# Kernel tuning notes

Measured on AMD Instinct MI355X. Metric: run time of the kernel, lower is better.

## Reference

```python
import jax, jax.numpy as jnp
import numpy as np

LN_EPS = 1e-5

def _layernorm(x, g, b):
    mu = jnp.mean(x, axis=-1, keepdims=True)
    var = jnp.mean(jnp.square(x - mu), axis=-1, keepdims=True)
    return (x - mu) * jax.lax.rsqrt(var + LN_EPS) * g + b

def setup_inputs() -> dict:
    key = jax.random.key(0)
    B, IN_DIM, S, D = 16384, 512, 32, 128
    ks = jax.random.split(key, 6)
    return {
        "x": jax.random.normal(ks[0], (B, IN_DIM), dtype=jnp.float32),
        "memory": jax.random.normal(ks[1], (1, S, D), dtype=jnp.float32),
        "ln_g": jnp.ones((IN_DIM,), dtype=jnp.float32),
        "ln_b": jnp.zeros((IN_DIM,), dtype=jnp.float32),
        "w_in": jax.random.normal(ks[2], (IN_DIM, D), dtype=jnp.float32) * 0.02,
        "b_in": jnp.zeros((D,), dtype=jnp.float32),
        "w_gate": jax.random.normal(ks[3], (2 * D, D), dtype=jnp.float32) * 0.02,
        "b_gate": jnp.zeros((D,), dtype=jnp.float32),
    }

def reference(x, memory, ln_g, ln_b, w_in, b_in, w_gate, b_gate):
    B = x.shape[0]
    mem = memory[0]                                   # [S, D]
    S, D = mem.shape
    x_proj = _layernorm(x, ln_g, ln_b) @ w_in + b_in  # [B, D]
    scores = x_proj @ mem.T                           # [B, S]
    probs = jax.nn.softmax(scores, axis=-1)           # [B, S]
    # read path
    read_content = probs @ mem                        # [B, D]
    # write path
    mem_b = jnp.broadcast_to(mem, (B, S, D))
    xp_b = jnp.broadcast_to(x_proj[:, None, :], (B, S, D))
    gate_in = jnp.concatenate([mem_b, xp_b], axis=-1)              # [B, S, 2D]
    update_gate = jax.nn.sigmoid(gate_in @ w_gate + b_gate)        # [B, S, D]
    write_info = probs[:, :, None] * x_proj[:, None, :]            # [B, S, D]
    avg_gate = jnp.mean(update_gate, axis=0, keepdims=True)        # [1, S, D]
    avg_write = jnp.mean(write_info, axis=0, keepdims=True)        # [1, S, D]
    new_memory = memory * (1.0 - avg_gate) + avg_write * avg_gate  # [1, S, D]
    return read_content, jax.lax.stop_gradient(new_memory)
```

## Files before the change

kernel.cpp:

```cpp
#include <hip/hip_runtime.h>
#include <hip/hip_bf16.h>
#include <stdint.h>

typedef __attribute__((ext_vector_type(8))) short bfrag_t;
typedef __attribute__((ext_vector_type(4))) float floatx4;
typedef __attribute__((ext_vector_type(8))) unsigned short ushort8_t;

#define WFRAG_OFF   0
#define GB_OFF      294912
#define BU_OFF      311296
#define BS_OFF      311808
#define MEMFRAG_OFF 311936
#define ACC_OFF     327680
#define NBLK        512

#define M_A     0
#define M_XPF   32768
#define M_U     40960
#define M_SC    57344
#define M_PR    61440
#define M_PRT   63488
#define M_LDS   65536

__device__ __forceinline__ unsigned short f2bf(float f) {
    union { __hip_bfloat16 b; unsigned short u; } cv;
    cv.b = __float2bfloat16(f);
    return cv.u;
}
__device__ __forceinline__ float bf2f(unsigned short h) {
    return __uint_as_float(((unsigned)h) << 16);
}
__device__ __forceinline__ void writefrag(unsigned short* wf, int k, int n, float v) {
    int kt = k >> 5, kk = k & 31;
    int lane = (n & 15) | ((kk >> 3) << 4);
    wf[(((kt * 18) + (n >> 4)) * 64 + lane) * 8 + (kk & 7)] = f2bf(v);
}

__global__ __launch_bounds__(256) void prep_kernel(
    const float* __restrict__ memv, const float* __restrict__ w_in,
    const float* __restrict__ b_in, const float* __restrict__ w_gate,
    const float* __restrict__ b_gate, unsigned char* __restrict__ ws)
{
    int bid = blockIdx.x, t = threadIdx.x;
    unsigned short* wfrag = (unsigned short*)(ws + WFRAG_OFF);
    const float* wg2 = w_gate + 128 * 128;

    if (bid < 256) {
        __shared__ float wrow[2][128];
        int k0 = bid * 2;
        wrow[t >> 7][t & 127] = w_in[(size_t)(k0 + (t >> 7)) * 128 + (t & 127)];
        __syncthreads();
        for (int kl = 0; kl < 2; ++kl) {
            int k = k0 + kl;
            float v;
            if (t < 128) {
                v = wrow[kl][t];
            } else {
                int d = t - 128;
                float acc = 0.f;
                #pragma unroll 16
                for (int j = 0; j < 128; ++j) acc += wrow[kl][j] * wg2[j * 128 + d];
                v = acc;
            }
            writefrag(wfrag, k, t, v);
            if (t < 32) {
                float acc = 0.f;
                #pragma unroll 16
                for (int d = 0; d < 128; ++d) acc += wrow[kl][d] * memv[t * 128 + d];
                writefrag(wfrag, k, 256 + t, acc);
            }
        }
    } else if (bid < 272) {
        int idx = (bid - 256) * 256 + t;
        int s = idx >> 7, d = idx & 127;
        float acc = b_gate[d];
        #pragma unroll 16
        for (int k = 0; k < 128; ++k) acc += memv[s * 128 + k] * w_gate[k * 128 + d];
        ((float*)(ws + GB_OFF))[idx] = acc;
    } else {
        if (t < 128) {
            float acc = 0.f;
            #pragma unroll 16
            for (int j = 0; j < 128; ++j) acc += b_in[j] * wg2[j * 128 + t];
            ((float*)(ws + BU_OFF))[t] = acc;
        }
        if (t < 32) {
            float acc = 0.f;
            #pragma unroll 16
            for (int d = 0; d < 128; ++d) acc += b_in[d] * memv[t * 128 + d];
            ((float*)(ws + BS_OFF))[t] = acc;
        }
        unsigned short* mfr = (unsigned short*)(ws + MEMFRAG_OFF);
        for (int idx = t; idx < 4096; idx += 256) {
            int s = idx >> 7, d = idx & 127;
            mfr[((d >> 4) * 64 + ((d & 15) | (((s >> 3) & 3) << 4))) * 8 + (s & 7)]
                = f2bf(memv[idx]);
        }
    }
}

__global__ __launch_bounds__(512, 4) void main_kernel(
    const float* __restrict__ x,
    const float* __restrict__ ln_g, const float* __restrict__ ln_b,
    const float* __restrict__ b_in, unsigned char* __restrict__ ws,
    float* __restrict__ out)
{
    __shared__ char smem[M_LDS] __attribute__((aligned(16)));

    int tid = threadIdx.x;
    int w = tid >> 6, l = tid & 63;
    int lane_lo = l & 15, lane_hi = l >> 4;
    int row_base = blockIdx.x * 32;

    int nf = (w < 2) ? 3 : 2;
    int nts[3] = {w, w + 8, 16 + w};
    const bfrag_t* wf = (const bfrag_t*)(ws + WFRAG_OFF);

    const float4* x4 = (const float4*)x;
    float4 g0 = ((const float4*)ln_g)[l];
    float4 g1 = ((const float4*)ln_g)[l + 64];
    float4 q0 = ((const float4*)ln_b)[l];
    float4 q1 = ((const float4*)ln_b)[l + 64];

    float4 xa[4], xb[4];
    #pragma unroll
    for (int i = 0; i < 4; ++i) {
        int r = w * 4 + i;
        xa[i] = x4[(size_t)(row_base + r) * 128 + l];
        xb[i] = x4[(size_t)(row_base + r) * 128 + 64 + l];
    }

    bfrag_t bcur[3], bnxt[3], bfar[3];
    #pragma unroll
    for (int i = 0; i < 3; ++i) {
        if (i < nf) {
            bcur[i] = wf[(0 * 18 + nts[i]) * 64 + l];
            bnxt[i] = wf[(1 * 18 + nts[i]) * 64 + l];
        }
    }
    float bin_v = b_in[w * 16 + lane_lo];
    float bu_v  = ((const float*)(ws + BU_OFF))[w * 16 + lane_lo];
    float bs_v  = (w < 2) ? ((const float*)(ws + BS_OFF))[w * 16 + lane_lo] : 0.f;

    #pragma unroll
    for (int i = 0; i < 4; ++i) {
        int r = w * 4 + i;
        float s1 = xa[i].x + xa[i].y + xa[i].z + xa[i].w + xb[i].x + xb[i].y + xb[i].z + xb[i].w;
        float s2 = xa[i].x*xa[i].x + xa[i].y*xa[i].y + xa[i].z*xa[i].z + xa[i].w*xa[i].w
                 + xb[i].x*xb[i].x + xb[i].y*xb[i].y + xb[i].z*xb[i].z + xb[i].w*xb[i].w;
        #pragma unroll
        for (int m = 1; m < 64; m <<= 1) {
            s1 += __shfl_xor(s1, m);
            s2 += __shfl_xor(s2, m);
        }
        float mu = s1 * (1.f / 512.f);
        float var = s2 * (1.f / 512.f) - mu * mu;
        float rs = rsqrtf(var + 1e-5f);
        float ya0 = (xa[i].x - mu) * rs * g0.x + q0.x;
        float ya1 = (xa[i].y - mu) * rs * g0.y + q0.y;
        float ya2 = (xa[i].z - mu) * rs * g0.z + q0.z;
        float ya3 = (xa[i].w - mu) * rs * g0.w + q0.w;
        float yb0 = (xb[i].x - mu) * rs * g1.x + q1.x;
        float yb1 = (xb[i].y - mu) * rs * g1.y + q1.y;
        float yb2 = (xb[i].z - mu) * rs * g1.z + q1.z;
        float yb3 = (xb[i].w - mu) * rs * g1.w + q1.w;
        unsigned long long pa =
            (unsigned long long)f2bf(ya0) | ((unsigned long long)f2bf(ya1) << 16) |
            ((unsigned long long)f2bf(ya2) << 32) | ((unsigned long long)f2bf(ya3) << 48);
        unsigned long long pb =
            (unsigned long long)f2bf(yb0) | ((unsigned long long)f2bf(yb1) << 16) |
            ((unsigned long long)f2bf(yb2) << 32) | ((unsigned long long)f2bf(yb3) << 48);
        int sw = (r & 7) << 4;
        *(unsigned long long*)(smem + M_A + ((r * 1024 + l * 8) ^ sw)) = pa;
        *(unsigned long long*)(smem + M_A + ((r * 1024 + 512 + l * 8) ^ sw)) = pb;
    }
    __syncthreads();

    int swa = (l & 7) << 4;
    int ab0 = lane_lo * 1024 + (lane_hi << 4);
    int ab1 = (16 + lane_lo) * 1024 + (lane_hi << 4);

    floatx4 acc[3][2];
    #pragma unroll
    for (int i = 0; i < 3; ++i)
        #pragma unroll
        for (int mt = 0; mt < 2; ++mt)
            acc[i][mt] = (floatx4){0.f, 0.f, 0.f, 0.f};

    bfrag_t acur0, acur1, anxt0, anxt1, afar0, afar1;
    acur0 = *(const bfrag_t*)(smem + M_A + (ab0 ^ swa));
    acur1 = *(const bfrag_t*)(smem + M_A + (ab1 ^ swa));
    anxt0 = *(const bfrag_t*)(smem + M_A + ((ab0 + 64) ^ swa));
    anxt1 = *(const bfrag_t*)(smem + M_A + ((ab1 + 64) ^ swa));

    for (int kt = 0; kt < 16; ++kt) {
        if (kt < 14) {
            int ko = (kt + 2) * 64;
            afar0 = *(const bfrag_t*)(smem + M_A + ((ab0 + ko) ^ swa));
            afar1 = *(const bfrag_t*)(smem + M_A + ((ab1 + ko) ^ swa));
            #pragma unroll
            for (int i = 0; i < 3; ++i)
                if (i < nf) bfar[i] = wf[((kt + 2) * 18 + nts[i]) * 64 + l];
        }
        #pragma unroll
        for (int i = 0; i < 3; ++i) {
            if (i < nf) {
                acc[i][0] = __builtin_amdgcn_mfma_f32_16x16x32_bf16(acur0, bcur[i], acc[i][0], 0, 0, 0);
                acc[i][1] = __builtin_amdgcn_mfma_f32_16x16x32_bf16(acur1, bcur[i], acc[i][1], 0, 0, 0);
            }
        }
        acur0 = anxt0; acur1 = anxt1; anxt0 = afar0; anxt1 = afar1;
        #pragma unroll
        for (int i = 0; i < 3; ++i)
            if (i < nf) { bcur[i] = bnxt[i]; bnxt[i] = bfar[i]; }
    }

    {
        #pragma unroll
        for (int i = 0; i < 3; ++i) {
            if (i < nf) {
                int n = nts[i] * 16 + lane_lo;
                float bias = (i == 0) ? bin_v : ((i == 1) ? bu_v : bs_v);
                #pragma unroll
                for (int mt = 0; mt < 2; ++mt) {
                    #pragma unroll
                    for (int r4 = 0; r4 < 4; ++r4) {
                        int row = mt * 16 + lane_hi * 4 + r4;
                        float v = acc[i][mt][r4] + bias;
                        if (i == 0) {
                            int addr = M_XPF +
                                (((n >> 4) * 64 + ((n & 15) | ((row >> 3) << 4))) * 8
                                 + (row & 7)) * 2;
                            *(unsigned short*)(smem + addr) = f2bf(v);
                        } else if (i == 1) {
                            int d = n - 128;
                            *(float*)(smem + M_U + (row * 128 + d) * 4) = __expf(-v);
                        } else {
                            int s = n - 256;
                            *(float*)(smem + M_SC + (row * 32 + s) * 4) = v;
                        }
                    }
                }
            }
        }
    }
    __syncthreads();

    bfrag_t bm = ((const bfrag_t*)(ws + MEMFRAG_OFF))[w * 64 + l];
    bfrag_t bx = *(const bfrag_t*)(smem + M_XPF + (w * 64 + l) * 16);
    int sbase = w * 4;
    const float* gb = (const float*)(ws + GB_OFF);
    float gbr0[4], gbr1[4];
    #pragma unroll
    for (int si = 0; si < 4; ++si) {
        gbr0[si] = gb[(sbase + si) * 128 + l];
        gbr1[si] = gb[(sbase + si) * 128 + l + 64];
    }

    #pragma unroll
    for (int i = 0; i < 4; ++i) {
        int r = w * 4 + i;
        int s = l & 31;
        float sc = *(const float*)(smem + M_SC + (r * 32 + s) * 4);
        float mx = sc;
        #pragma unroll
        for (int m = 1; m < 32; m <<= 1) mx = fmaxf(mx, __shfl_xor(mx, m));
        float e = __expf(sc - mx);
        float sum = e;
        #pragma unroll
        for (int m = 1; m < 32; m <<= 1) sum += __shfl_xor(sum, m);
        float p = e * __builtin_amdgcn_rcpf(sum);
        if (l < 32) {
            unsigned short pb = f2bf(p);
            *(unsigned short*)(smem + M_PR +
                (((r >> 4) * 64 + ((r & 15) + 16 * (s >> 3))) * 8 + (s & 7)) * 2) = pb;
            *(unsigned short*)(smem + M_PRT +
                (((s >> 4) * 64 + ((s & 15) + 16 * (r >> 3))) * 8 + (r & 7)) * 2) = pb;
        }
    }
    __syncthreads();

    unsigned short* pwh = (unsigned short*)(ws + ACC_OFF + (size_t)blockIdx.x * 16384);
    {
        bfrag_t pa0 = *(const bfrag_t*)(smem + M_PR + l * 16);
        bfrag_t pa1 = *(const bfrag_t*)(smem + M_PR + 1024 + l * 16);
        bfrag_t pat0 = *(const bfrag_t*)(smem + M_PRT + l * 16);
        bfrag_t pat1 = *(const bfrag_t*)(smem + M_PRT + 1024 + l * 16);

        floatx4 r0 = (floatx4){0.f, 0.f, 0.f, 0.f};
        floatx4 r1 = (floatx4){0.f, 0.f, 0.f, 0.f};
        r0 = __builtin_amdgcn_mfma_f32_16x16x32_bf16(pa0, bm, r0, 0, 0, 0);
        r1 = __builtin_amdgcn_mfma_f32_16x16x32_bf16(pa1, bm, r1, 0, 0, 0);
        floatx4 w0 = (floatx4){0.f, 0.f, 0.f, 0.f};
        floatx4 w1 = (floatx4){0.f, 0.f, 0.f, 0.f};
        w0 = __builtin_amdgcn_mfma_f32_16x16x32_bf16(pat0, bx, w0, 0, 0, 0);
        w1 = __builtin_amdgcn_mfma_f32_16x16x32_bf16(pat1, bx, w1, 0, 0, 0);

        int nc = w * 16 + lane_lo;
        #pragma unroll
        for (int r4 = 0; r4 < 4; ++r4) {
            int row = lane_hi * 4 + r4;
            out[(size_t)(row_base + row) * 128 + nc] = r0[r4];
            out[(size_t)(row_base + row + 16) * 128 + nc] = r1[r4];
            pwh[row * 128 + nc] = f2bf(w0[r4]);
            pwh[(row + 16) * 128 + nc] = f2bf(w1[r4]);
        }
    }

    {
        unsigned short* pgh = pwh + 4096;
        float En0[4], En1[4], ag0[4], ag1[4];
        #pragma unroll
        for (int si = 0; si < 4; ++si) {
            En0[si] = __expf(-gbr0[si]);
            En1[si] = __expf(-gbr1[si]);
            ag0[si] = 0.f; ag1[si] = 0.f;
        }
        #pragma unroll 4
        for (int r = 0; r < 32; ++r) {
            float eu0 = *(const float*)(smem + M_U + (r * 128 + l) * 4);
            float eu1 = *(const float*)(smem + M_U + (r * 128 + l + 64) * 4);
            #pragma unroll
            for (int si = 0; si < 4; ++si) {
                ag0[si] += __builtin_amdgcn_rcpf(1.f + En0[si] * eu0);
                ag1[si] += __builtin_amdgcn_rcpf(1.f + En1[si] * eu1);
            }
        }
        #pragma unroll
        for (int si = 0; si < 4; ++si) {
            pgh[(sbase + si) * 128 + l]      = f2bf(ag0[si]);
            pgh[(sbase + si) * 128 + l + 64] = f2bf(ag1[si]);
        }
    }
}

__global__ __launch_bounds__(512) void fin_kernel(
    const float* __restrict__ memv, const unsigned char* __restrict__ ws,
    float* __restrict__ out2)
{
    __shared__ float red[8][8][8];
    __shared__ float fsum[64];
    int b = blockIdx.x, t = threadIdx.x;
    int wv = t >> 6, l = t & 63;
    int sub = t & 7;
    int arr = sub >> 2, q = sub & 3;

    const unsigned char* base = ws + ACC_OFF;
    float v[8];
    #pragma unroll
    for (int i = 0; i < 8; ++i) v[i] = 0.f;

    #pragma unroll
    for (int j = 0; j < 8; ++j) {
        int copy = j * 64 + (t >> 3);
        ushort8_t u = *(const ushort8_t*)(base + (size_t)copy * 16384 + arr * 8192
                                          + b * 64 + q * 16);
        #pragma unroll
        for (int i = 0; i < 8; ++i) v[i] += bf2f(u[i]);
    }
    #pragma unroll
    for (int m = 8; m < 64; m <<= 1) {
        #pragma unroll
        for (int i = 0; i < 8; ++i) v[i] += __shfl_xor(v[i], m);
    }
    if (l < 8) {
        #pragma unroll
        for (int i = 0; i < 8; ++i) red[wv][l][i] = v[i];
    }
    __syncthreads();
    if (t < 64) {
        int sb = t >> 3, k = t & 7;
        float s = 0.f;
        #pragma unroll
        for (int c = 0; c < 8; ++c) s += red[c][sb][k];
        fsum[(sb >> 2) * 32 + (sb & 3) * 8 + k] = s;
    }
    __syncthreads();
    if (t < 32) {
        float a = fsum[t] * (1.f / 16384.f);
        float g = fsum[32 + t] * (1.f / 16384.f);
        int e = b * 32 + t;
        out2[e] = memv[e] * (1.f - g) + a * g;
    }
}

extern "C" void kernel_launch(void* const* d_in, const int* in_sizes, int n_in,
                              void* d_out, int out_size, void* d_ws, size_t ws_size,
                              hipStream_t stream)
{
    (void)in_sizes; (void)n_in; (void)out_size; (void)ws_size;
    const float* x      = (const float*)d_in[0];
    const float* memv   = (const float*)d_in[1];
    const float* ln_g   = (const float*)d_in[2];
    const float* ln_b   = (const float*)d_in[3];
    const float* w_in   = (const float*)d_in[4];
    const float* b_in   = (const float*)d_in[5];
    const float* w_gate = (const float*)d_in[6];
    const float* b_gate = (const float*)d_in[7];
    float* out = (float*)d_out;
    unsigned char* ws = (unsigned char*)d_ws;

    hipLaunchKernelGGL(prep_kernel, dim3(273), dim3(256), 0, stream,
                       memv, w_in, b_in, w_gate, b_gate, ws);
    hipLaunchKernelGGL(main_kernel, dim3(NBLK), dim3(512), 0, stream,
                       x, ln_g, ln_b, b_in, ws, out);
    hipLaunchKernelGGL(fin_kernel, dim3(128), dim3(512), 0, stream,
                       memv, ws, out + 2097152);
}
```

Baseline: 41.57 us.

## Defer layernorm normalization past the GEMM using precomputed gamma/beta projections

Instead of normalizing each row before the projection GEMM, the kernel stores x*gamma in bf16 and applies the per-row rstd and mean corrections after the MFMA accumulation, using column vectors W^T·gamma and W^T·beta+bias precomputed in an extra prep block. The row statistics reductions are batched across the four rows so shuffles interleave, and only lane 0 writes rstd and rstd*mu to shared memory. This takes the mean reduction off the critical path before the LDS stores and removes the per-element normalize math. It also raises precision risk, because the un-centered x is quantized to bf16 and the mean is subtracted afterwards, which can cancel badly.

```diff
diff --git a/kernel.cpp b/kernel.cpp
--- a/kernel.cpp
+++ b/kernel.cpp
@@ -8,9 +8,9 @@
 
 #define WFRAG_OFF   0
 #define GB_OFF      294912
-#define BU_OFF      311296
-#define BS_OFF      311808
-#define MEMFRAG_OFF 311936
+#define G_OFF       311296
+#define QB_OFF      312448
+#define MEMFRAG_OFF 313600
 #define ACC_OFF     327680
 #define NBLK        512
 
@@ -39,7 +39,8 @@
 __global__ __launch_bounds__(256) void prep_kernel(
     const float* __restrict__ memv, const float* __restrict__ w_in,
     const float* __restrict__ b_in, const float* __restrict__ w_gate,
-    const float* __restrict__ b_gate, unsigned char* __restrict__ ws)
+    const float* __restrict__ b_gate, const float* __restrict__ ln_g,
+    const float* __restrict__ ln_b, unsigned char* __restrict__ ws)
 {
     int bid = blockIdx.x, t = threadIdx.x;
     unsigned short* wfrag = (unsigned short*)(ws + WFRAG_OFF);
@@ -77,33 +78,59 @@
         #pragma unroll 16
         for (int k = 0; k < 128; ++k) acc += memv[s * 128 + k] * w_gate[k * 128 + d];
         ((float*)(ws + GB_OFF))[idx] = acc;
-    } else {
-        if (t < 128) {
-            float acc = 0.f;
-            #pragma unroll 16
-            for (int j = 0; j < 128; ++j) acc += b_in[j] * wg2[j * 128 + t];
-            ((float*)(ws + BU_OFF))[t] = acc;
-        }
-        if (t < 32) {
-            float acc = 0.f;
-            #pragma unroll 16
-            for (int d = 0; d < 128; ++d) acc += b_in[d] * memv[t * 128 + d];
-            ((float*)(ws + BS_OFF))[t] = acc;
-        }
+    } else if (bid == 272) {
         unsigned short* mfr = (unsigned short*)(ws + MEMFRAG_OFF);
         for (int idx = t; idx < 4096; idx += 256) {
             int s = idx >> 7, d = idx & 127;
             mfr[((d >> 4) * 64 + ((d & 15) | (((s >> 3) & 3) << 4))) * 8 + (s & 7)]
                 = f2bf(memv[idx]);
         }
+    } else {
+        __shared__ float tt[128], uu[128];
+        float* G  = (float*)(ws + G_OFF);
+        float* QB = (float*)(ws + QB_OFF);
+        if (t < 128) {
+            float at = 0.f, au = 0.f;
+            #pragma unroll 8
+            for (int k = 0; k < 512; ++k) {
+                float wv = w_in[(size_t)k * 128 + t];
+                at += ln_g[k] * wv;
+                au += ln_b[k] * wv;
+            }
+            tt[t] = at;
+            uu[t] = au + b_in[t];
+        }
+        __syncthreads();
+        if (t < 128) {
+            G[t]  = tt[t];
+            QB[t] = uu[t];
+            float ag = 0.f, aq = 0.f;
+            #pragma unroll 16
+            for (int j = 0; j < 128; ++j) {
+                float wv = wg2[j * 128 + t];
+                ag += tt[j] * wv;
+                aq += uu[j] * wv;
+            }
+            G[128 + t]  = ag;
+            QB[128 + t] = aq;
+        } else if (t < 160) {
+            int s = t - 128;
+            float ag = 0.f, aq = 0.f;
+            #pragma unroll 16
+            for (int d = 0; d < 128; ++d) {
+                float mv = memv[s * 128 + d];
+                ag += tt[d] * mv;
+                aq += uu[d] * mv;
+            }
+            G[256 + s]  = ag;
+            QB[256 + s] = aq;
+        }
     }
 }
 
 __global__ __launch_bounds__(512, 4) void main_kernel(
-    const float* __restrict__ x,
-    const float* __restrict__ ln_g, const float* __restrict__ ln_b,
-    const float* __restrict__ b_in, unsigned char* __restrict__ ws,
-    float* __restrict__ out)
+    const float* __restrict__ x, const float* __restrict__ ln_g,
+    unsigned char* __restrict__ ws, float* __restrict__ out)
 {
     __shared__ char smem[M_LDS] __attribute__((aligned(16)));
 
@@ -115,12 +142,12 @@
     int nf = (w < 2) ? 3 : 2;
     int nts[3] = {w, w + 8, 16 + w};
     const bfrag_t* wf = (const bfrag_t*)(ws + WFRAG_OFF);
+    float* rsA = (float*)(smem + M_PR);
+    float* rmA = (float*)(smem + M_PR + 128);
 
     const float4* x4 = (const float4*)x;
     float4 g0 = ((const float4*)ln_g)[l];
     float4 g1 = ((const float4*)ln_g)[l + 64];
-    float4 q0 = ((const float4*)ln_b)[l];
-    float4 q1 = ((const float4*)ln_b)[l + 64];
 
     float4 xa[4], xb[4];
     #pragma unroll
@@ -138,32 +165,24 @@
             bnxt[i] = wf[(1 * 18 + nts[i]) * 64 + l];
         }
     }
-    float bin_v = b_in[w * 16 + lane_lo];
-    float bu_v  = ((const float*)(ws + BU_OFF))[w * 16 + lane_lo];
-    float bs_v  = (w < 2) ? ((const float*)(ws + BS_OFF))[w * 16 + lane_lo] : 0.f;
-
+    float Gv[3], QBv[3];
+    #pragma unroll
+    for (int i = 0; i < 3; ++i) {
+        if (i < nf) {
+            int n = nts[i] * 16 + lane_lo;
+            Gv[i]  = ((const float*)(ws + G_OFF))[n];
+            QBv[i] = ((const float*)(ws + QB_OFF))[n];
+        }
+    }
+
+    float s1v[4], s2v[4];
     #pragma unroll
     for (int i = 0; i < 4; ++i) {
         int r = w * 4 + i;
-        float s1 = xa[i].x + xa[i].y + xa[i].z + xa[i].w + xb[i].x + xb[i].y + xb[i].z + xb[i].w;
-        float s2 = xa[i].x*xa[i].x + xa[i].y*xa[i].y + xa[i].z*xa[i].z + xa[i].w*xa[i].w
-                 + xb[i].x*xb[i].x + xb[i].y*xb[i].y + xb[i].z*xb[i].z + xb[i].w*xb[i].w;
-        #pragma unroll
-        for (int m = 1; m < 64; m <<= 1) {
-            s1 += __shfl_xor(s1, m);
-            s2 += __shfl_xor(s2, m);
-        }
-        float mu = s1 * (1.f / 512.f);
-        float var = s2 * (1.f / 512.f) - mu * mu;
-        float rs = rsqrtf(var + 1e-5f);
-        float ya0 = (xa[i].x - mu) * rs * g0.x + q0.x;
-        float ya1 = (xa[i].y - mu) * rs * g0.y + q0.y;
-        float ya2 = (xa[i].z - mu) * rs * g0.z + q0.z;
-        float ya3 = (xa[i].w - mu) * rs * g0.w + q0.w;
-        float yb0 = (xb[i].x - mu) * rs * g1.x + q1.x;
-        float yb1 = (xb[i].y - mu) * rs * g1.y + q1.y;
-        float yb2 = (xb[i].z - mu) * rs * g1.z + q1.z;
-        float yb3 = (xb[i].w - mu) * rs * g1.w + q1.w;
+        float ya0 = xa[i].x * g0.x, ya1 = xa[i].y * g0.y;
+        float ya2 = xa[i].z * g0.z, ya3 = xa[i].w * g0.w;
+        float yb0 = xb[i].x * g1.x, yb1 = xb[i].y * g1.y;
+        float yb2 = xb[i].z * g1.z, yb3 = xb[i].w * g1.w;
         unsigned long long pa =
             (unsigned long long)f2bf(ya0) | ((unsigned long long)f2bf(ya1) << 16) |
             ((unsigned long long)f2bf(ya2) << 32) | ((unsigned long long)f2bf(ya3) << 48);
@@ -173,6 +192,28 @@
         int sw = (r & 7) << 4;
         *(unsigned long long*)(smem + M_A + ((r * 1024 + l * 8) ^ sw)) = pa;
         *(unsigned long long*)(smem + M_A + ((r * 1024 + 512 + l * 8) ^ sw)) = pb;
+        s1v[i] = xa[i].x + xa[i].y + xa[i].z + xa[i].w + xb[i].x + xb[i].y + xb[i].z + xb[i].w;
+        s2v[i] = xa[i].x*xa[i].x + xa[i].y*xa[i].y + xa[i].z*xa[i].z + xa[i].w*xa[i].w
+               + xb[i].x*xb[i].x + xb[i].y*xb[i].y + xb[i].z*xb[i].z + xb[i].w*xb[i].w;
+    }
+    #pragma unroll
+    for (int m = 1; m < 64; m <<= 1) {
+        #pragma unroll
+        for (int i = 0; i < 4; ++i) {
+            s1v[i] += __shfl_xor(s1v[i], m);
+            s2v[i] += __shfl_xor(s2v[i], m);
+        }
+    }
+    if (l == 0) {
+        #pragma unroll
+        for (int i = 0; i < 4; ++i) {
+            int r = w * 4 + i;
+            float mu = s1v[i] * (1.f / 512.f);
+            float var = s2v[i] * (1.f / 512.f) - mu * mu;
+            float rs = rsqrtf(var + 1e-5f);
+            rsA[r] = rs;
+            rmA[r] = rs * mu;
+        }
     }
     __syncthreads();
 
@@ -216,17 +257,26 @@
     }
 
     {
+        float rsv[8], rmv[8];
+        #pragma unroll
+        for (int mt = 0; mt < 2; ++mt)
+            #pragma unroll
+            for (int r4 = 0; r4 < 4; ++r4) {
+                int row = mt * 16 + lane_hi * 4 + r4;
+                rsv[mt * 4 + r4] = rsA[row];
+                rmv[mt * 4 + r4] = rmA[row];
+            }
         #pragma unroll
         for (int i = 0; i < 3; ++i) {
             if (i < nf) {
                 int n = nts[i] * 16 + lane_lo;
-                float bias = (i == 0) ? bin_v : ((i == 1) ? bu_v : bs_v);
                 #pragma unroll
                 for (int mt = 0; mt < 2; ++mt) {
                     #pragma unroll
                     for (int r4 = 0; r4 < 4; ++r4) {
                         int row = mt * 16 + lane_hi * 4 + r4;
-                        float v = acc[i][mt][r4] + bias;
+                        float base = QBv[i] - rmv[mt * 4 + r4] * Gv[i];
+                        float v = rsv[mt * 4 + r4] * acc[i][mt][r4] + base;
                         if (i == 0) {
                             int addr = M_XPF +
                                 (((n >> 4) * 64 + ((n & 15) | ((row >> 3) << 4))) * 8
@@ -400,10 +450,10 @@
     float* out = (float*)d_out;
     unsigned char* ws = (unsigned char*)d_ws;
 
-    hipLaunchKernelGGL(prep_kernel, dim3(273), dim3(256), 0, stream,
-                       memv, w_in, b_in, w_gate, b_gate, ws);
+    hipLaunchKernelGGL(prep_kernel, dim3(274), dim3(256), 0, stream,
+                       memv, w_in, b_in, w_gate, b_gate, ln_g, ln_b, ws);
     hipLaunchKernelGGL(main_kernel, dim3(NBLK), dim3(512), 0, stream,
-                       x, ln_g, ln_b, b_in, ws, out);
+                       x, ln_g, ws, out);
     hipLaunchKernelGGL(fin_kernel, dim3(128), dim3(512), 0, stream,
                        memv, ws, out + 2097152);
 }
```

After: 56.55 us. 36.0% more time.
